# Kernel tuning notes

Measured on AMD Instinct MI355X. Metric: run time of the kernel, lower is better.

Reference implementation:

```python
import jax, jax.numpy as jnp
import numpy as np

N_EMBED = 384
N_HEAD = 6
HEAD_DIM = N_EMBED // N_HEAD


def setup_inputs() -> dict:
    key = jax.random.key(0)
    k1, k2, k3 = jax.random.split(key, 3)
    B, T = 128, 256
    x = jax.random.normal(k1, (B, T, N_EMBED), dtype=jnp.float32)
    # nn.Linear(N_EMBED, 3*N_EMBED, bias=False): weight [3*N_EMBED, N_EMBED],
    # applied as x @ W.T -> store transposed [N_EMBED, 3*N_EMBED]
    W_qkv = jax.random.normal(k2, (N_EMBED, 3 * N_EMBED), dtype=jnp.float32) * (N_EMBED ** -0.5)
    W_proj = jax.random.normal(k3, (N_EMBED, N_EMBED), dtype=jnp.float32) * (N_EMBED ** -0.5)
    return {"x": x, "W_qkv": W_qkv, "W_proj": W_proj}


def reference(x, W_qkv, W_proj):
    B, T, C = x.shape
    qkv = jnp.einsum('btc,cd->btd', x, W_qkv)  # [B,T,3C]
    q, k, v = jnp.split(qkv, 3, axis=-1)
    # [B, H, T, Dh]
    q = q.reshape(B, T, N_HEAD, HEAD_DIM).transpose(0, 2, 1, 3)
    k = k.reshape(B, T, N_HEAD, HEAD_DIM).transpose(0, 2, 1, 3)
    v = v.reshape(B, T, N_HEAD, HEAD_DIM).transpose(0, 2, 1, 3)
    scale = HEAD_DIM ** -0.5
    wei = jnp.einsum('bhqd,bhkd->bhqk', q, k) * scale  # [B,H,T,T]
    causal = jnp.tril(jnp.ones((T, T), dtype=bool))
    wei = jnp.where(causal[None, None, :, :], wei, -jnp.inf)
    wei = jax.nn.softmax(wei, axis=-1)
    # dropout layers are identity in eval mode
    out = jnp.einsum('bhqk,bhkd->bhqd', wei, v)  # [B,H,T,Dh]
    out = out.transpose(0, 2, 1, 3).reshape(B, T, C)
    out = jnp.einsum('btc,cd->btd', out, W_proj)
    return out
```

## Files before the change

### kernel.cpp

```cpp
#include <hip/hip_runtime.h>
#include <hip/hip_bf16.h>

typedef __attribute__((ext_vector_type(8))) short short8;
typedef __attribute__((ext_vector_type(4))) float f32x4;
typedef __attribute__((ext_vector_type(4))) unsigned short ush4;

typedef const __attribute__((address_space(1))) void* gas_p;
typedef __attribute__((address_space(3))) void* las_p;
#define GLOAD_LDS16(g, l) __builtin_amdgcn_global_load_lds((gas_p)(const void*)(g), (las_p)(void*)(l), 16, 0, 0)

__device__ __forceinline__ unsigned short f2bf(float f) {
    union { float f; unsigned int u; } v; v.f = f;
    unsigned int r = v.u + 0x7FFFu + ((v.u >> 16) & 1u);
    return (unsigned short)(r >> 16);
}
__device__ __forceinline__ unsigned pk2(float a, float b) {
    return (unsigned)f2bf(a) | ((unsigned)f2bf(b) << 16);
}

__global__ __launch_bounds__(256) void cast_x_kernel(
    const float* __restrict__ x, unsigned short* __restrict__ xb, int n8)
{
    int i = blockIdx.x * 256 + threadIdx.x;
    if (i >= n8) return;
    const float4* p = (const float4*)x + (size_t)i * 2;
    float4 a = p[0], b = p[1];
    short8 o;
    o[0] = (short)f2bf(a.x); o[1] = (short)f2bf(a.y);
    o[2] = (short)f2bf(a.z); o[3] = (short)f2bf(a.w);
    o[4] = (short)f2bf(b.x); o[5] = (short)f2bf(b.y);
    o[6] = (short)f2bf(b.z); o[7] = (short)f2bf(b.w);
    *(short8*)(xb + (size_t)i * 8) = o;
}

__global__ __launch_bounds__(256) void cast_wt_kernel(
    const float* __restrict__ W, unsigned short* __restrict__ Wt, int K, int N)
{
    int idx = blockIdx.x * 256 + threadIdx.x;
    if (idx >= N * K) return;
    int n = idx / K, k = idx - n * K;
    Wt[idx] = f2bf(W[(size_t)k * N + n]);
}

__global__ __launch_bounds__(256, 2) void gemm_qkv_kernel(
    const unsigned short* __restrict__ A,
    const unsigned short* __restrict__ Bt,
    unsigned short* __restrict__ qkb,
    unsigned short* __restrict__ vtb)
{
    const int K = 384;
    __shared__ __align__(16) unsigned short As[256 * 64];
    __shared__ __align__(16) unsigned short Bs[128 * 64];
    const int tid = threadIdx.x;
    const int lane = tid & 63, wv = tid >> 6;
    const int c = lane & 15, g = lane >> 4;
    const int wm = (wv >> 1) * 128, wn = (wv & 1) * 64;

    const int mpx = 16;
    const int id = blockIdx.x, xcd = id & 7, kk = id >> 3;
    const long m0 = (long)(xcd * mpx + (kk % mpx)) * 256;
    const long n0 = (long)(kk / mpx) * 128;

    f32x4 acc[8][4] = {};
    const int xr = (c & 7) << 4;

    for (int kt = 0; kt < K; kt += 64) {
        #pragma unroll
        for (int i = 0; i < 8; ++i) {
            int ch = i * 256 + tid;
            int row = ch >> 3, cc = ch & 7;
            GLOAD_LDS16(&A[(m0 + row) * (size_t)K + kt + (cc ^ (row & 7)) * 8],
                        &As[(i * 256 + wv * 64) * 8]);
        }
        #pragma unroll
        for (int i = 0; i < 4; ++i) {
            int ch = i * 256 + tid;
            int row = ch >> 3, cc = ch & 7;
            GLOAD_LDS16(&Bt[(n0 + row) * (size_t)K + kt + (cc ^ (row & 7)) * 8],
                        &Bs[(i * 256 + wv * 64) * 8]);
        }
        __syncthreads();
        #pragma unroll
        for (int ks = 0; ks < 2; ++ks) {
            short8 bf_[4];
            #pragma unroll
            for (int i = 0; i < 4; ++i)
                bf_[i] = *(const short8*)((char*)Bs +
                    (((wn + i * 16 + c) * 128 + (ks * 32 + g * 8) * 2) ^ xr));
            #pragma unroll
            for (int mi = 0; mi < 8; ++mi) {
                short8 af = *(const short8*)((char*)As +
                    (((wm + mi * 16 + c) * 128 + (ks * 32 + g * 8) * 2) ^ xr));
                #pragma unroll
                for (int ni = 0; ni < 4; ++ni)
                    acc[mi][ni] = __builtin_amdgcn_mfma_f32_16x16x32_bf16(
                        af, bf_[ni], acc[mi][ni], 0, 0, 0);
            }
        }
        __syncthreads();
    }

    if (n0 < 768) {
        #pragma unroll
        for (int mi = 0; mi < 8; ++mi)
            #pragma unroll
            for (int ni = 0; ni < 4; ++ni)
                #pragma unroll
                for (int r = 0; r < 4; ++r) {
                    long m = m0 + wm + mi * 16 + g * 4 + r;
                    long n = n0 + wn + ni * 16 + c;
                    qkb[m * 768 + n] = f2bf(acc[mi][ni][r]);
                }
    } else {
        char* wbase = (char*)As + wv * 8192;
        const int h = (int)((n0 + wn - 768) >> 6);
        const long b = (m0 + wm) >> 8;
        const int tb = (int)((m0 + wm) & 255);
        const long bh = b * 6 + h;
        #pragma unroll
        for (int mh = 0; mh < 2; ++mh) {
            #pragma unroll
            for (int ni = 0; ni < 4; ++ni)
                #pragma unroll
                for (int mq = 0; mq < 4; ++mq)
                    #pragma unroll
                    for (int r = 0; r < 4; ++r) {
                        int d = ni * 16 + c, t = mq * 16 + g * 4 + r;
                        int byte = (d * 128 + t * 2) ^ ((d & 7) << 4);
                        *(unsigned short*)(wbase + byte) = f2bf(acc[mh * 4 + mq][ni][r]);
                    }
            __asm__ __volatile__("" ::: "memory");
            #pragma unroll
            for (int it = 0; it < 8; ++it) {
                int d = it * 8 + (lane >> 3), ck = lane & 7;
                short8 v = *(const short8*)(wbase + ((d * 128 + ck * 16) ^ ((d & 7) << 4)));
                *(short8*)&vtb[(bh * 64 + d) * 256 + tb + mh * 64 + ck * 8] = v;
            }
            __asm__ __volatile__("" ::: "memory");
        }
    }
}

__global__ __launch_bounds__(256, 2) void gemm_proj_kernel(
    const unsigned short* __restrict__ A, const unsigned short* __restrict__ Bt,
    float* __restrict__ C, int M, int N, int K)
{
    __shared__ __align__(16) unsigned short As[128 * 64];
    __shared__ __align__(16) unsigned short Bs[128 * 64];
    const int tid = threadIdx.x;
    const int lane = tid & 63, wv = tid >> 6;
    const int c = lane & 15, g = lane >> 4;
    const int wm = (wv >> 1) * 64, wn = (wv & 1) * 64;

    const int mpx = (M >> 7) >> 3;
    const int id = blockIdx.x, xcd = id & 7, kk = id >> 3;
    const long m0 = (long)(xcd * mpx + (kk % mpx)) * 128;
    const long n0 = (long)(kk / mpx) * 128;

    f32x4 acc[4][4] = {};
    const int xr = (c & 7) << 4;

    for (int kt = 0; kt < K; kt += 64) {
        #pragma unroll
        for (int i = 0; i < 4; ++i) {
            int ch = i * 256 + wv * 64 + lane;
            int row = ch >> 3, cc = ch & 7;
            int sc = (cc ^ (row & 7)) * 8;
            GLOAD_LDS16(&A[(m0 + row) * (size_t)K + kt + sc],
                        &As[(i * 256 + wv * 64) * 8]);
            GLOAD_LDS16(&Bt[(n0 + row) * (size_t)K + kt + sc],
                        &Bs[(i * 256 + wv * 64) * 8]);
        }
        __syncthreads();
        #pragma unroll
        for (int ks = 0; ks < 2; ++ks) {
            short8 af[4], bf_[4];
            #pragma unroll
            for (int i = 0; i < 4; ++i)
                af[i] = *(const short8*)((char*)As +
                    (((wm + i * 16 + c) * 128 + (ks * 32 + g * 8) * 2) ^ xr));
            #pragma unroll
            for (int i = 0; i < 4; ++i)
                bf_[i] = *(const short8*)((char*)Bs +
                    (((wn + i * 16 + c) * 128 + (ks * 32 + g * 8) * 2) ^ xr));
            #pragma unroll
            for (int mi = 0; mi < 4; ++mi)
                #pragma unroll
                for (int ni = 0; ni < 4; ++ni)
                    acc[mi][ni] = __builtin_amdgcn_mfma_f32_16x16x32_bf16(
                        af[mi], bf_[ni], acc[mi][ni], 0, 0, 0);
        }
        __syncthreads();
    }

    #pragma unroll
    for (int mi = 0; mi < 4; ++mi)
        #pragma unroll
        for (int ni = 0; ni < 4; ++ni)
            #pragma unroll
            for (int r = 0; r < 4; ++r) {
                long m = m0 + wm + mi * 16 + g * 4 + r;
                long n = n0 + wn + ni * 16 + c;
                C[m * N + n] = acc[mi][ni][r];
            }
}

__global__ __launch_bounds__(256, 3) void attn_kernel(
    const unsigned short* __restrict__ qk,
    const unsigned short* __restrict__ vt,
    unsigned short* __restrict__ outp)
{
    const int bh = blockIdx.x;
    const int b = bh / 6, h = bh - b * 6;
    const int tid = threadIdx.x;
    const int lane = tid & 63, wv = tid >> 6;
    const int c = lane & 15, g = lane >> 4;

    __shared__ unsigned short Ks[256 * 64];
    __shared__ unsigned short Pl[4][16 * 64];

    #pragma unroll
    for (int it = 0; it < 8; ++it) {
        int ch = it * 256 + tid;
        int row = ch >> 3, col = (ch & 7) * 8;
        int db = (row * 128 + col * 2) ^ ((row & 7) << 4);
        *(short8*)((char*)Ks + db) =
            *(const short8*)&qk[(size_t)(b * 256 + row) * 768 + 384 + h * 64 + col];
    }
    __syncthreads();

    char* plw = (char*)Pl[wv];

    for (int t = 0; t < 2; ++t) {
        const int p = t ? 7 - wv : wv;
        const int jlast = p >> 1;
        const int modd = (p & 1) * 32;
        const int qt0 = p * 32;

        short8 aq[2][2];
        #pragma unroll
        for (int mi = 0; mi < 2; ++mi)
            #pragma unroll
            for (int ks = 0; ks < 2; ++ks)
                aq[mi][ks] = *(const short8*)&qk[
                    (size_t)(b * 256 + qt0 + mi * 16 + c) * 768 + h * 64 + ks * 32 + g * 8];

        f32x4 o[2][4] = {};
        float mrun[2] = {-1e30f, -1e30f}, lrun[2] = {0.f, 0.f};

        for (int j = 0; j <= jlast; ++j) {
            short8 bv[4][2];
            #pragma unroll
            for (int nd = 0; nd < 4; ++nd)
                #pragma unroll
                for (int ks = 0; ks < 2; ++ks)
                    bv[nd][ks] = *(const short8*)&vt[
                        ((size_t)bh * 64 + nd * 16 + c) * 256 + j * 64 + ks * 32 + g * 8];

            short8 bk[4][2];
            #pragma unroll
            for (int ni = 0; ni < 4; ++ni)
                #pragma unroll
                for (int ks = 0; ks < 2; ++ks) {
                    int key = j * 64 + ni * 16 + c;
                    bk[ni][ks] = *(const short8*)((char*)Ks +
                        ((key * 128 + (ks * 32 + g * 8) * 2) ^ ((key & 7) << 4)));
                }

            #pragma unroll
            for (int mi = 0; mi < 2; ++mi) {
                float pv[4][4];
                #pragma unroll
                for (int ni = 0; ni < 4; ++ni) {
                    f32x4 z = {0.f, 0.f, 0.f, 0.f};
                    z = __builtin_amdgcn_mfma_f32_16x16x32_bf16(bk[ni][0], aq[mi][0], z, 0, 0, 0);
                    z = __builtin_amdgcn_mfma_f32_16x16x32_bf16(bk[ni][1], aq[mi][1], z, 0, 0, 0);
                    #pragma unroll
                    for (int r = 0; r < 4; ++r) {
                        float v = z[r] * 0.125f;
                        if (j == jlast) {
                            int kloc = ni * 16 + g * 4 + r;
                            int qloc = mi * 16 + c + modd;
                            if (kloc > qloc) v = -1e30f;
                        }
                        pv[ni][r] = v;
                    }
                }
                float m01 = fmaxf(fmaxf(pv[0][0], pv[0][1]), fmaxf(pv[0][2], pv[0][3]));
                float m11 = fmaxf(fmaxf(pv[1][0], pv[1][1]), fmaxf(pv[1][2], pv[1][3]));
                float m21 = fmaxf(fmaxf(pv[2][0], pv[2][1]), fmaxf(pv[2][2], pv[2][3]));
                float m31 = fmaxf(fmaxf(pv[3][0], pv[3][1]), fmaxf(pv[3][2], pv[3][3]));
                float m1 = fmaxf(fmaxf(m01, m11), fmaxf(m21, m31));
                m1 = fmaxf(m1, __shfl_xor(m1, 16));
                m1 = fmaxf(m1, __shfl_xor(m1, 32));
                float mold = mrun[mi];
                float mnew = fmaxf(mold, m1);
                float fac = __expf(mold - mnew);
                float ssum = 0.f;
                #pragma unroll
                for (int ni = 0; ni < 4; ++ni)
                    #pragma unroll
                    for (int r = 0; r < 4; ++r) {
                        float pp = __expf(pv[ni][r] - mnew);
                        pv[ni][r] = pp;
                        ssum += pp;
                    }
                ssum += __shfl_xor(ssum, 16);
                ssum += __shfl_xor(ssum, 32);
                lrun[mi] = lrun[mi] * fac + ssum;
                mrun[mi] = mnew;
                #pragma unroll
                for (int nd = 0; nd < 4; ++nd)
                    #pragma unroll
                    for (int r = 0; r < 4; ++r) o[mi][nd][r] *= fac;

                __asm__ __volatile__("" ::: "memory");
                #pragma unroll
                for (int ni = 0; ni < 4; ++ni) {
                    uint2 w;
                    w.x = pk2(pv[ni][0], pv[ni][1]);
                    w.y = pk2(pv[ni][2], pv[ni][3]);
                    *(uint2*)(plw + ((c * 128 + ni * 32 + g * 8) ^ ((c & 7) << 4))) = w;
                }
                __asm__ __volatile__("" ::: "memory");

                short8 ap[2];
                #pragma unroll
                for (int ks = 0; ks < 2; ++ks)
                    ap[ks] = *(const short8*)(plw +
                        ((c * 128 + ks * 64 + g * 16) ^ ((c & 7) << 4)));

                #pragma unroll
                for (int nd = 0; nd < 4; ++nd) {
                    o[mi][nd] = __builtin_amdgcn_mfma_f32_16x16x32_bf16(bv[nd][0], ap[0], o[mi][nd], 0, 0, 0);
                    o[mi][nd] = __builtin_amdgcn_mfma_f32_16x16x32_bf16(bv[nd][1], ap[1], o[mi][nd], 0, 0, 0);
                }
                __asm__ __volatile__("" ::: "memory");
            }
        }

        #pragma unroll
        for (int mi = 0; mi < 2; ++mi) {
            float inv = 1.0f / lrun[mi];
            #pragma unroll
            for (int nd = 0; nd < 4; ++nd) {
                ush4 w;
                #pragma unroll
                for (int r = 0; r < 4; ++r) w[r] = f2bf(o[mi][nd][r] * inv);
                *(ush4*)&outp[((size_t)b * 256 + qt0 + mi * 16 + c) * 384 + h * 64 + nd * 16 + g * 4] = w;
            }
        }
    }
}

extern "C" void kernel_launch(void* const* d_in, const int* in_sizes, int n_in,
                              void* d_out, int out_size, void* d_ws, size_t ws_size,
                              hipStream_t stream) {
    const float* x     = (const float*)d_in[0];
    const float* Wqkv  = (const float*)d_in[1];
    const float* Wproj = (const float*)d_in[2];

    char* ws = (char*)d_ws;
    unsigned short* xb     = (unsigned short*)(ws);
    unsigned short* wqkvt  = (unsigned short*)(ws + 25165824);
    unsigned short* wprojt = (unsigned short*)(ws + 26050560);
    unsigned short* qkb    = (unsigned short*)(ws + 26345472);
    unsigned short* vtb    = (unsigned short*)(ws + 76677120);
    unsigned short* attnb  = (unsigned short*)(ws + 101842944);

    cast_x_kernel<<<6144, 256, 0, stream>>>(x, xb, 1572864);
    cast_wt_kernel<<<1728, 256, 0, stream>>>(Wqkv, wqkvt, 384, 1152);
    cast_wt_kernel<<<576, 256, 0, stream>>>(Wproj, wprojt, 384, 384);

    gemm_qkv_kernel<<<1152, 256, 0, stream>>>(xb, wqkvt, qkb, vtb);
    attn_kernel<<<768, 256, 0, stream>>>(qkb, vtb, attnb);
    gemm_proj_kernel<<<768, 256, 0, stream>>>(attnb, wprojt, (float*)d_out, 32768, 384, 384);
}
```

Baseline: 119.0 us.

## Fuse fp32-to-bf16 cast of x into QKV GEMM and shrink tile to 128x128

```diff
diff --git a/kernel.cpp b/kernel.cpp
--- a/kernel.cpp
+++ b/kernel.cpp
@@ -16,21 +16,6 @@
 }
 __device__ __forceinline__ unsigned pk2(float a, float b) {
     return (unsigned)f2bf(a) | ((unsigned)f2bf(b) << 16);
-}
-
-__global__ __launch_bounds__(256) void cast_x_kernel(
-    const float* __restrict__ x, unsigned short* __restrict__ xb, int n8)
-{
-    int i = blockIdx.x * 256 + threadIdx.x;
-    if (i >= n8) return;
-    const float4* p = (const float4*)x + (size_t)i * 2;
-    float4 a = p[0], b = p[1];
-    short8 o;
-    o[0] = (short)f2bf(a.x); o[1] = (short)f2bf(a.y);
-    o[2] = (short)f2bf(a.z); o[3] = (short)f2bf(a.w);
-    o[4] = (short)f2bf(b.x); o[5] = (short)f2bf(b.y);
-    o[6] = (short)f2bf(b.z); o[7] = (short)f2bf(b.w);
-    *(short8*)(xb + (size_t)i * 8) = o;
 }
 
 __global__ __launch_bounds__(256) void cast_wt_kernel(
@@ -43,35 +28,28 @@
 }
 
 __global__ __launch_bounds__(256, 2) void gemm_qkv_kernel(
-    const unsigned short* __restrict__ A,
+    const float* __restrict__ x,
     const unsigned short* __restrict__ Bt,
     unsigned short* __restrict__ qkb,
     unsigned short* __restrict__ vtb)
 {
     const int K = 384;
-    __shared__ __align__(16) unsigned short As[256 * 64];
-    __shared__ __align__(16) unsigned short Bs[128 * 64];
+    __shared__ __align__(16) unsigned short Sh[2 * 128 * 64];
+    unsigned short* As = Sh;
+    unsigned short* Bs = Sh + 128 * 64;
     const int tid = threadIdx.x;
     const int lane = tid & 63, wv = tid >> 6;
     const int c = lane & 15, g = lane >> 4;
-    const int wm = (wv >> 1) * 128, wn = (wv & 1) * 64;
-
-    const int mpx = 16;
+    const int wm = (wv >> 1) * 64, wn = (wv & 1) * 64;
+
     const int id = blockIdx.x, xcd = id & 7, kk = id >> 3;
-    const long m0 = (long)(xcd * mpx + (kk % mpx)) * 256;
-    const long n0 = (long)(kk / mpx) * 128;
-
-    f32x4 acc[8][4] = {};
+    const long m0 = (long)(xcd * 32 + kk / 9) * 128;
+    const long n0 = (long)(kk % 9) * 128;
+
+    f32x4 acc[4][4] = {};
     const int xr = (c & 7) << 4;
 
     for (int kt = 0; kt < K; kt += 64) {
-        #pragma unroll
-        for (int i = 0; i < 8; ++i) {
-            int ch = i * 256 + tid;
-            int row = ch >> 3, cc = ch & 7;
-            GLOAD_LDS16(&A[(m0 + row) * (size_t)K + kt + (cc ^ (row & 7)) * 8],
-                        &As[(i * 256 + wv * 64) * 8]);
-        }
         #pragma unroll
         for (int i = 0; i < 4; ++i) {
             int ch = i * 256 + tid;
@@ -79,30 +57,43 @@
             GLOAD_LDS16(&Bt[(n0 + row) * (size_t)K + kt + (cc ^ (row & 7)) * 8],
                         &Bs[(i * 256 + wv * 64) * 8]);
         }
+        #pragma unroll
+        for (int i = 0; i < 4; ++i) {
+            int ch = i * 256 + tid;
+            int row = ch >> 3, cc = ch & 7;
+            const float* ga = &x[(m0 + row) * (size_t)K + kt + (cc ^ (row & 7)) * 8];
+            float4 a = *(const float4*)ga;
+            float4 b = *(const float4*)(ga + 4);
+            uint4 w;
+            w.x = pk2(a.x, a.y); w.y = pk2(a.z, a.w);
+            w.z = pk2(b.x, b.y); w.w = pk2(b.z, b.w);
+            *(uint4*)&As[ch * 8] = w;
+        }
         __syncthreads();
         #pragma unroll
         for (int ks = 0; ks < 2; ++ks) {
-            short8 bf_[4];
+            short8 af[4], bf_[4];
+            #pragma unroll
+            for (int i = 0; i < 4; ++i)
+                af[i] = *(const short8*)((char*)As +
+                    (((wm + i * 16 + c) * 128 + (ks * 32 + g * 8) * 2) ^ xr));
             #pragma unroll
             for (int i = 0; i < 4; ++i)
                 bf_[i] = *(const short8*)((char*)Bs +
                     (((wn + i * 16 + c) * 128 + (ks * 32 + g * 8) * 2) ^ xr));
             #pragma unroll
-            for (int mi = 0; mi < 8; ++mi) {
-                short8 af = *(const short8*)((char*)As +
-                    (((wm + mi * 16 + c) * 128 + (ks * 32 + g * 8) * 2) ^ xr));
+            for (int mi = 0; mi < 4; ++mi)
                 #pragma unroll
                 for (int ni = 0; ni < 4; ++ni)
                     acc[mi][ni] = __builtin_amdgcn_mfma_f32_16x16x32_bf16(
-                        af, bf_[ni], acc[mi][ni], 0, 0, 0);
-            }
+                        af[mi], bf_[ni], acc[mi][ni], 0, 0, 0);
         }
         __syncthreads();
     }
 
     if (n0 < 768) {
         #pragma unroll
-        for (int mi = 0; mi < 8; ++mi)
+        for (int mi = 0; mi < 4; ++mi)
             #pragma unroll
             for (int ni = 0; ni < 4; ++ni)
                 #pragma unroll
@@ -112,31 +103,27 @@
                     qkb[m * 768 + n] = f2bf(acc[mi][ni][r]);
                 }
     } else {
-        char* wbase = (char*)As + wv * 8192;
-        const int h = (int)((n0 + wn - 768) >> 6);
-        const long b = (m0 + wm) >> 8;
-        const int tb = (int)((m0 + wm) & 255);
-        const long bh = b * 6 + h;
-        #pragma unroll
-        for (int mh = 0; mh < 2; ++mh) {
-            #pragma unroll
-            for (int ni = 0; ni < 4; ++ni)
-                #pragma unroll
-                for (int mq = 0; mq < 4; ++mq)
-                    #pragma unroll
-                    for (int r = 0; r < 4; ++r) {
-                        int d = ni * 16 + c, t = mq * 16 + g * 4 + r;
-                        int byte = (d * 128 + t * 2) ^ ((d & 7) << 4);
-                        *(unsigned short*)(wbase + byte) = f2bf(acc[mh * 4 + mq][ni][r]);
-                    }
-            __asm__ __volatile__("" ::: "memory");
-            #pragma unroll
-            for (int it = 0; it < 8; ++it) {
-                int d = it * 8 + (lane >> 3), ck = lane & 7;
-                short8 v = *(const short8*)(wbase + ((d * 128 + ck * 16) ^ ((d & 7) << 4)));
-                *(short8*)&vtb[(bh * 64 + d) * 256 + tb + mh * 64 + ck * 8] = v;
-            }
-            __asm__ __volatile__("" ::: "memory");
+        char* wbase = (char*)Sh + wv * 8192;
+        #pragma unroll
+        for (int ni = 0; ni < 4; ++ni)
+            #pragma unroll
+            for (int mi = 0; mi < 4; ++mi)
+                #pragma unroll
+                for (int r = 0; r < 4; ++r) {
+                    int d = ni * 16 + c, t = mi * 16 + g * 4 + r;
+                    int byte = (d * 128 + t * 2) ^ ((d & 7) << 4);
+                    *(unsigned short*)(wbase + byte) = f2bf(acc[mi][ni][r]);
+                }
+        __asm__ __volatile__("" ::: "memory");
+        int h = (int)((n0 + wn - 768) >> 6);
+        long b = (m0 + wm) >> 8;
+        int t0 = (int)((m0 + wm) & 255);
+        long bh = b * 6 + h;
+        #pragma unroll
+        for (int it = 0; it < 8; ++it) {
+            int d = it * 8 + (lane >> 3), ck = lane & 7;
+            short8 v = *(const short8*)(wbase + ((d * 128 + ck * 16) ^ ((d & 7) << 4)));
+            *(short8*)&vtb[(bh * 64 + d) * 256 + t0 + ck * 8] = v;
         }
     }
 }
@@ -361,18 +348,16 @@
     const float* Wproj = (const float*)d_in[2];
 
     char* ws = (char*)d_ws;
-    unsigned short* xb     = (unsigned short*)(ws);
-    unsigned short* wqkvt  = (unsigned short*)(ws + 25165824);
-    unsigned short* wprojt = (unsigned short*)(ws + 26050560);
-    unsigned short* qkb    = (unsigned short*)(ws + 26345472);
-    unsigned short* vtb    = (unsigned short*)(ws + 76677120);
-    unsigned short* attnb  = (unsigned short*)(ws + 101842944);
-
-    cast_x_kernel<<<6144, 256, 0, stream>>>(x, xb, 1572864);
+    unsigned short* wqkvt  = (unsigned short*)(ws);
+    unsigned short* wprojt = (unsigned short*)(ws + 884736);
+    unsigned short* qkb    = (unsigned short*)(ws + 1179648);
+    unsigned short* vtb    = (unsigned short*)(ws + 51511296);
+    unsigned short* attnb  = (unsigned short*)(ws + 76677120);
+
     cast_wt_kernel<<<1728, 256, 0, stream>>>(Wqkv, wqkvt, 384, 1152);
     cast_wt_kernel<<<576, 256, 0, stream>>>(Wproj, wprojt, 384, 384);
 
-    gemm_qkv_kernel<<<1152, 256, 0, stream>>>(xb, wqkvt, qkb, vtb);
+    gemm_qkv_kernel<<<2304, 256, 0, stream>>>(x, wqkvt, qkb, vtb);
     attn_kernel<<<768, 256, 0, stream>>>(qkb, vtb, attnb);
     gemm_proj_kernel<<<768, 256, 0, stream>>>(attnb, wprojt, (float*)d_out, 32768, 384, 384);
 }
```

New measurement: 125.1 us. 1.05x slower.
